# Optimization experiments

Measured on AMD Instinct MI355X. Metric: run time of the kernel, lower is better.

The kernel has to match this reference:

```python
import jax, jax.numpy as jnp
import numpy as np

D = 256; NH = 8; NL = 4; NP = 4; HD = D // NH
SHAPES = np.array([[64, 64], [32, 32], [16, 16], [8, 8]], dtype=np.int32)  # (H, W) per level
LSI = np.array([0, 4096, 5120, 5376], dtype=np.int32)
B = 4; LQ = int(SHAPES.prod(axis=1).sum())  # 5440


def setup_inputs() -> dict:
    key = jax.random.key(0)
    ks = jax.random.split(key, 16)
    p = lambda i, shape, s=0.02: jax.random.normal(ks[i], shape, dtype=jnp.float32) * s
    return dict(
        src=jax.random.normal(ks[0], (B, LQ, D), dtype=jnp.float32),
        pos=jax.random.normal(ks[1], (B, LQ, D), dtype=jnp.float32),
        reference_points=jax.random.uniform(ks[2], (B, LQ, NL, 2), dtype=jnp.float32),
        spatial_shapes=jnp.asarray(SHAPES),
        level_start_index=jnp.asarray(LSI),
        Wv=p(3, (D, D)), bv=jnp.zeros((D,), jnp.float32),
        Woff=p(4, (D, NH * NL * NP * 2)), boff=p(5, (NH * NL * NP * 2,)),
        Wattn=p(6, (D, NH * NL * NP)), battn=p(7, (NH * NL * NP,)),
        Wout=p(8, (D, D)), bout=jnp.zeros((D,), jnp.float32),
        g1=jnp.ones((D,), jnp.float32), b1=jnp.zeros((D,), jnp.float32),
        W1=p(9, (D, D)), bb1=jnp.zeros((D,), jnp.float32),
        W2=p(10, (D, D)), bb2=jnp.zeros((D,), jnp.float32),
        g3=jnp.ones((D,), jnp.float32), b3=jnp.zeros((D,), jnp.float32),
    )


def _ln(x, g, b, eps=1e-5):
    m = jnp.mean(x, -1, keepdims=True)
    v = jnp.mean(jnp.square(x - m), -1, keepdims=True)
    return (x - m) * jax.lax.rsqrt(v + eps) * g + b


def _bilinear(vflat, Hl, Wl, loc):
    # vflat: [B, Hl*Wl, nh, hd]; loc: [B, Lq, nh, np, 2] normalized to [0,1]
    # align_corners=False, zero padding (matches F.grid_sample in MSDeformAttn)
    x = loc[..., 0] * Wl - 0.5
    y = loc[..., 1] * Hl - 0.5
    x0 = jnp.floor(x); y0 = jnp.floor(y)
    fx = x - x0; fy = y - y0
    x0 = x0.astype(jnp.int32); y0 = y0.astype(jnp.int32)
    Bb, Lq, nh, npnt = x0.shape
    hd = vflat.shape[-1]
    out = jnp.zeros((Bb, Lq, nh, npnt, hd), vflat.dtype)
    for dy in (0, 1):
        for dx in (0, 1):
            xi = x0 + dx; yi = y0 + dy
            w = (fx if dx else 1.0 - fx) * (fy if dy else 1.0 - fy)
            valid = (xi >= 0) & (xi < Wl) & (yi >= 0) & (yi < Hl)
            idx = jnp.clip(yi, 0, Hl - 1) * Wl + jnp.clip(xi, 0, Wl - 1)  # [B,Lq,nh,np]
            idx = idx.transpose(0, 1, 3, 2).reshape(Bb, Lq * npnt, nh, 1)
            g = jnp.take_along_axis(vflat, idx, axis=1)
            g = g.reshape(Bb, Lq, npnt, nh, hd).transpose(0, 1, 3, 2, 4)
            out = out + g * (w * valid.astype(w.dtype))[..., None]
    return out  # [B, Lq, nh, np, hd]


def _forward(src, pos, reference_points, spatial_shapes, level_start_index,
             Wv, bv, Woff, boff, Wattn, battn, Wout, bout,
             g1, b1, W1, bb1, W2, bb2, g3, b3):
    shapes = np.asarray(spatial_shapes)
    lsi = np.asarray(level_start_index)
    Bq, Lq, Dm = src.shape
    q = src + pos  # with_pos_embed
    value = (src @ Wv + bv).reshape(Bq, Lq, NH, HD)
    off = (q @ Woff + boff).reshape(Bq, Lq, NH, NL, NP, 2)
    aw = jax.nn.softmax((q @ Wattn + battn).reshape(Bq, Lq, NH, NL * NP), axis=-1)
    aw = aw.reshape(Bq, Lq, NH, NL, NP)
    # offset normalizer is (W, H) per level
    norm = jnp.stack([shapes[:, 1].astype(np.float32), shapes[:, 0].astype(np.float32)], axis=-1)
    loc = reference_points[:, :, None, :, None, :] + off / norm[None, None, None, :, None, :]
    attended = jnp.zeros((Bq, Lq, NH, HD), src.dtype)
    for l in range(shapes.shape[0]):
        Hl, Wl = int(shapes[l, 0]), int(shapes[l, 1])
        s = int(lsi[l])
        vflat = value[:, s:s + Hl * Wl]
        sampled = _bilinear(vflat, Hl, Wl, loc[:, :, :, l])  # [B,Lq,nh,np,hd]
        attended = attended + jnp.einsum('blhpd,blhp->blhd', sampled, aw[:, :, :, l])
    src2 = attended.reshape(Bq, Lq, Dm) @ Wout + bout
    # residual + LayerNorm (dropout is identity in eval)
    sxy = _ln(src + src2, g1, b1)
    # FFN (d_ffn == d_model here), residual + LayerNorm
    h = jax.nn.relu(sxy @ W1 + bb1)
    return _ln(sxy + (h @ W2 + bb2), g3, b3)


def reference(src, pos, reference_points, spatial_shapes, level_start_index,
              Wv, bv, Woff, boff, Wattn, battn, Wout, bout,
              g1, b1, W1, bb1, W2, bb2, g3, b3):
    return _forward(src, pos, reference_points, spatial_shapes, level_start_index,
                    Wv, bv, Woff, boff, Wattn, battn, Wout, bout,
                    g1, b1, W1, bb1, W2, bb2, g3, b3)
```

## Files before the change

### kernel.cpp

```cpp
#include <hip/hip_runtime.h>
#include <cstddef>
#include <cstdint>

#define M_TOK 21760
#define LQ_ 5440

typedef _Float16 f16x8 __attribute__((ext_vector_type(8)));
typedef _Float16 h2v __attribute__((ext_vector_type(2)));
typedef float f32x4v __attribute__((ext_vector_type(4)));
typedef _Float16 half4v __attribute__((ext_vector_type(4)));

__device__ __forceinline__ unsigned short f2h(float f) {
  return __builtin_bit_cast(unsigned short, (_Float16)f);
}

__global__ __launch_bounds__(256) void prep_k(
    const float* __restrict__ src, const float* __restrict__ pos,
    const float* __restrict__ Wv, const float* __restrict__ Woff,
    const float* __restrict__ Wattn, const float* __restrict__ Wout,
    const float* __restrict__ W1, const float* __restrict__ W2,
    unsigned short* __restrict__ s16, unsigned short* __restrict__ q16,
    unsigned short* __restrict__ G)
{
  const int b = blockIdx.x;
  if (b < 5440) {
    const int i = b * 256 + threadIdx.x;
    const float4 s = ((const float4*)src)[i];
    const float4 p = ((const float4*)pos)[i];
    ushort4 a, q;
    a.x = f2h(s.x); a.y = f2h(s.y); a.z = f2h(s.z); a.w = f2h(s.w);
    q.x = f2h(s.x + p.x); q.y = f2h(s.y + p.y); q.z = f2h(s.z + p.z); q.w = f2h(s.w + p.w);
    ((ushort4*)s16)[i] = a;
    ((ushort4*)q16)[i] = q;
  } else {
    const int gid = (b - 5440) * 256 + threadIdx.x;
    const float* srcs[6] = {Wv, Woff, Wattn, Wout, W1, W2};
    const int starts[7] = {0, 65536, 131072, 163840, 229376, 294912, 360448};
    const int Nn[6] = {256, 256, 128, 256, 256, 256};
    int m = 0;
#pragma unroll
    for (int i = 1; i < 6; ++i) m += (gid >= starts[i]);
    const int local = gid - starts[m];
    const int n = local >> 8;
    const int k = local & 255;
    G[gid] = f2h(srcs[m][(size_t)k * Nn[m] + n]);
  }
}

__global__ __launch_bounds__(256, 2) void gemm_qkv_k(
    const unsigned short* __restrict__ s16, const unsigned short* __restrict__ q16,
    const unsigned short* __restrict__ WvT, const unsigned short* __restrict__ WfT,
    const float* __restrict__ bv, const float* __restrict__ boff,
    const float* __restrict__ battn,
    unsigned short* __restrict__ value16, unsigned short* __restrict__ fused16)
{
  const int by = blockIdx.y;
  const bool isv = (by < 2);
  const unsigned short* A  = isv ? s16 : q16;
  const unsigned short* Wt = isv ? WvT : WfT;
  const int n0 = isv ? by * 128 : (by - 2) * 128;
  const int N  = isv ? 256 : 384;
  unsigned short* out16 = isv ? value16 : fused16;
  const float* bsel; int nsub;
  if (isv)            { bsel = bv;    nsub = 0; }
  else if (n0 < 256)  { bsel = boff;  nsub = 0; }
  else                { bsel = battn; nsub = 256; }

  __shared__ unsigned short As[128 * 64];
  __shared__ unsigned short Bs[128 * 64];
  const int t = threadIdx.x;
  const int lane = t & 63, wave = t >> 6;
  const int wm = wave >> 1, wn = wave & 1;
  const int m0 = blockIdx.x * 128;

  const int lrow = lane >> 3;
  const int pcol = (lane & 7) << 4;
  const int scol = pcol ^ (lrow << 4);

  f32x4v acc[4][4];
#pragma unroll
  for (int i = 0; i < 4; ++i)
#pragma unroll
    for (int j = 0; j < 4; ++j) acc[i][j] = (f32x4v){0.f, 0.f, 0.f, 0.f};

  const int fr = lane & 15;
  const int fkb = (lane >> 4) << 4;

  for (int k0 = 0; k0 < 256; k0 += 64) {
#pragma unroll
    for (int i = 0; i < 4; ++i) {
      const int row = wave * 32 + i * 8 + lrow;
      const unsigned short* g = A + (size_t)(m0 + row) * 256 + k0 + (scol >> 1);
      unsigned short* s = As + (wave * 32 + i * 8) * 64;
      __builtin_amdgcn_global_load_lds(
          (const __attribute__((address_space(1))) void*)g,
          (__attribute__((address_space(3))) void*)s, 16, 0, 0);
    }
#pragma unroll
    for (int i = 0; i < 4; ++i) {
      const int row = wave * 32 + i * 8 + lrow;
      const unsigned short* g = Wt + (size_t)(n0 + row) * 256 + k0 + (scol >> 1);
      unsigned short* s = Bs + (wave * 32 + i * 8) * 64;
      __builtin_amdgcn_global_load_lds(
          (const __attribute__((address_space(1))) void*)g,
          (__attribute__((address_space(3))) void*)s, 16, 0, 0);
    }
    __syncthreads();

    f16x8 af[4][2], bfr[4][2];
#pragma unroll
    for (int i = 0; i < 4; ++i) {
      const int row = wm * 64 + i * 16 + fr;
      const char* base = (const char*)As + row * 128;
#pragma unroll
      for (int kk = 0; kk < 2; ++kk)
        af[i][kk] = *(const f16x8*)(base + ((kk * 64 + fkb) ^ ((row & 7) << 4)));
    }
#pragma unroll
    for (int j = 0; j < 4; ++j) {
      const int row = wn * 64 + j * 16 + fr;
      const char* base = (const char*)Bs + row * 128;
#pragma unroll
      for (int kk = 0; kk < 2; ++kk)
        bfr[j][kk] = *(const f16x8*)(base + ((kk * 64 + fkb) ^ ((row & 7) << 4)));
    }
#pragma unroll
    for (int i = 0; i < 4; ++i)
#pragma unroll
      for (int j = 0; j < 4; ++j) {
        acc[i][j] = __builtin_amdgcn_mfma_f32_16x16x32_f16(af[i][0], bfr[j][0], acc[i][j], 0, 0, 0);
        acc[i][j] = __builtin_amdgcn_mfma_f32_16x16x32_f16(af[i][1], bfr[j][1], acc[i][j], 0, 0, 0);
      }
    __syncthreads();
  }

  const int fq = lane >> 4;
#pragma unroll
  for (int j = 0; j < 4; ++j) {
    const int n = n0 + wn * 64 + j * 16 + fr;
    const float bj = bsel[n - nsub];
#pragma unroll
    for (int i = 0; i < 4; ++i) {
#pragma unroll
      for (int r = 0; r < 4; ++r) {
        const int m = m0 + wm * 64 + i * 16 + fq * 4 + r;
        out16[(size_t)m * N + n] = f2h(acc[i][j][r] + bj);
      }
    }
  }
}

__global__ __launch_bounds__(256, 2) void gemm16_k(
    const unsigned short* __restrict__ A, const unsigned short* __restrict__ Wt,
    const float* __restrict__ bias, unsigned short* __restrict__ out16,
    int N, int relu)
{
  __shared__ unsigned short As[128 * 64];
  __shared__ unsigned short Bs[128 * 64];
  const int t = threadIdx.x;
  const int lane = t & 63, wave = t >> 6;
  const int wm = wave >> 1, wn = wave & 1;
  const int m0 = blockIdx.x * 128, n0 = blockIdx.y * 128;

  const int lrow = lane >> 3;
  const int pcol = (lane & 7) << 4;
  const int scol = pcol ^ (lrow << 4);

  f32x4v acc[4][4];
#pragma unroll
  for (int i = 0; i < 4; ++i)
#pragma unroll
    for (int j = 0; j < 4; ++j) acc[i][j] = (f32x4v){0.f, 0.f, 0.f, 0.f};

  const int fr = lane & 15;
  const int fkb = (lane >> 4) << 4;

  for (int k0 = 0; k0 < 256; k0 += 64) {
#pragma unroll
    for (int i = 0; i < 4; ++i) {
      const int row = wave * 32 + i * 8 + lrow;
      const unsigned short* g = A + (size_t)(m0 + row) * 256 + k0 + (scol >> 1);
      unsigned short* s = As + (wave * 32 + i * 8) * 64;
      __builtin_amdgcn_global_load_lds(
          (const __attribute__((address_space(1))) void*)g,
          (__attribute__((address_space(3))) void*)s, 16, 0, 0);
    }
#pragma unroll
    for (int i = 0; i < 4; ++i) {
      const int row = wave * 32 + i * 8 + lrow;
      const unsigned short* g = Wt + (size_t)(n0 + row) * 256 + k0 + (scol >> 1);
      unsigned short* s = Bs + (wave * 32 + i * 8) * 64;
      __builtin_amdgcn_global_load_lds(
          (const __attribute__((address_space(1))) void*)g,
          (__attribute__((address_space(3))) void*)s, 16, 0, 0);
    }
    __syncthreads();

    f16x8 af[4][2], bfr[4][2];
#pragma unroll
    for (int i = 0; i < 4; ++i) {
      const int row = wm * 64 + i * 16 + fr;
      const char* base = (const char*)As + row * 128;
#pragma unroll
      for (int kk = 0; kk < 2; ++kk)
        af[i][kk] = *(const f16x8*)(base + ((kk * 64 + fkb) ^ ((row & 7) << 4)));
    }
#pragma unroll
    for (int j = 0; j < 4; ++j) {
      const int row = wn * 64 + j * 16 + fr;
      const char* base = (const char*)Bs + row * 128;
#pragma unroll
      for (int kk = 0; kk < 2; ++kk)
        bfr[j][kk] = *(const f16x8*)(base + ((kk * 64 + fkb) ^ ((row & 7) << 4)));
    }
#pragma unroll
    for (int i = 0; i < 4; ++i)
#pragma unroll
      for (int j = 0; j < 4; ++j) {
        acc[i][j] = __builtin_amdgcn_mfma_f32_16x16x32_f16(af[i][0], bfr[j][0], acc[i][j], 0, 0, 0);
        acc[i][j] = __builtin_amdgcn_mfma_f32_16x16x32_f16(af[i][1], bfr[j][1], acc[i][j], 0, 0, 0);
      }
    __syncthreads();
  }

  const int fq = lane >> 4;
#pragma unroll
  for (int j = 0; j < 4; ++j) {
    const int n = n0 + wn * 64 + j * 16 + fr;
    const float bj = bias[n];
#pragma unroll
    for (int i = 0; i < 4; ++i) {
#pragma unroll
      for (int r = 0; r < 4; ++r) {
        const int m = m0 + wm * 64 + i * 16 + fq * 4 + r;
        float v = acc[i][j][r] + bj;
        if (relu) v = fmaxf(v, 0.f);
        out16[(size_t)m * N + n] = f2h(v);
      }
    }
  }
}

__global__ __launch_bounds__(512, 4) void gemm_ln_k(
    const unsigned short* __restrict__ A, const unsigned short* __restrict__ Wt,
    const float* __restrict__ bias, const float* __restrict__ res,
    const float* __restrict__ g, const float* __restrict__ b,
    float* __restrict__ outf, unsigned short* __restrict__ out16)
{
  __shared__ unsigned short As[32 * 64];
  __shared__ unsigned short Bs[256 * 64 + 288];
  const int t = threadIdx.x;
  const int lane = t & 63, wave = t >> 6;
  const int rt = wave & 1, cg = wave >> 1;
  const int m0 = blockIdx.x * 32;

  const int lrow = lane >> 3;
  const int pcol = (lane & 7) << 4;
  const int scol = pcol ^ (lrow << 4);

  f32x4v acc[4];
#pragma unroll
  for (int j = 0; j < 4; ++j) acc[j] = (f32x4v){0.f, 0.f, 0.f, 0.f};

  const int fr = lane & 15;
  const int fq = lane >> 4;
  const int fkb = fq << 4;

  for (int k0 = 0; k0 < 256; k0 += 64) {
    if (wave < 4) {
      const int row = wave * 8 + lrow;
      const unsigned short* gp = A + (size_t)(m0 + row) * 256 + k0 + (scol >> 1);
      unsigned short* s = As + (wave * 8) * 64;
      __builtin_amdgcn_global_load_lds(
          (const __attribute__((address_space(1))) void*)gp,
          (__attribute__((address_space(3))) void*)s, 16, 0, 0);
    }
#pragma unroll
    for (int i = 0; i < 4; ++i) {
      const int row = wave * 32 + i * 8 + lrow;
      const unsigned short* gp = Wt + (size_t)row * 256 + k0 + (scol >> 1);
      unsigned short* s = Bs + (wave * 32 + i * 8) * 64;
      __builtin_amdgcn_global_load_lds(
          (const __attribute__((address_space(1))) void*)gp,
          (__attribute__((address_space(3))) void*)s, 16, 0, 0);
    }
    __syncthreads();

    f16x8 af0, af1;
    {
      const int arow = rt * 16 + fr;
      const char* abase = (const char*)As + arow * 128;
      af0 = *(const f16x8*)(abase + ((0 + fkb) ^ ((arow & 7) << 4)));
      af1 = *(const f16x8*)(abase + ((64 + fkb) ^ ((arow & 7) << 4)));
    }
#pragma unroll
    for (int j = 0; j < 4; ++j) {
      const int brow = cg * 64 + j * 16 + fr;
      const char* bbase = (const char*)Bs + brow * 128;
      const f16x8 b0 = *(const f16x8*)(bbase + ((0 + fkb) ^ ((brow & 7) << 4)));
      const f16x8 b1 = *(const f16x8*)(bbase + ((64 + fkb) ^ ((brow & 7) << 4)));
      acc[j] = __builtin_amdgcn_mfma_f32_16x16x32_f16(af0, b0, acc[j], 0, 0, 0);
      acc[j] = __builtin_amdgcn_mfma_f32_16x16x32_f16(af1, b1, acc[j], 0, 0, 0);
    }
    __syncthreads();
  }

  float* Cs = (float*)Bs;
#pragma unroll
  for (int j = 0; j < 4; ++j) {
    const int col = cg * 64 + j * 16 + fr;
#pragma unroll
    for (int rr = 0; rr < 4; ++rr) {
      const int row = rt * 16 + fq * 4 + rr;
      Cs[row * 260 + col] = acc[j][rr];
    }
  }
  __syncthreads();

  const int lg = lane >> 4, li = lane & 15;
  const int row = wave * 4 + lg;
  const size_t rowoff = (size_t)(m0 + row) * 256;

  float4 v[4];
  float s = 0.f;
#pragma unroll
  for (int c4 = 0; c4 < 4; ++c4) {
    const int col = c4 * 64 + li * 4;
    float4 x = *(float4*)&Cs[row * 260 + col];
    const float4 bi = *(const float4*)&bias[col];
    const float4 rv = *(const float4*)&res[rowoff + col];
    x.x += bi.x + rv.x; x.y += bi.y + rv.y;
    x.z += bi.z + rv.z; x.w += bi.w + rv.w;
    v[c4] = x;
    s += x.x + x.y + x.z + x.w;
  }
#pragma unroll
  for (int o = 1; o < 16; o <<= 1) s += __shfl_xor(s, o);
  const float mean = s * (1.f / 256.f);
  float ss = 0.f;
#pragma unroll
  for (int c4 = 0; c4 < 4; ++c4) {
    const float d0 = v[c4].x - mean, d1 = v[c4].y - mean;
    const float d2 = v[c4].z - mean, d3 = v[c4].w - mean;
    ss += d0 * d0 + d1 * d1 + d2 * d2 + d3 * d3;
  }
#pragma unroll
  for (int o = 1; o < 16; o <<= 1) ss += __shfl_xor(ss, o);
  const float rstd = rsqrtf(ss * (1.f / 256.f) + 1e-5f);

#pragma unroll
  for (int c4 = 0; c4 < 4; ++c4) {
    const int col = c4 * 64 + li * 4;
    const float4 gv = *(const float4*)&g[col];
    const float4 bv = *(const float4*)&b[col];
    float4 o4;
    o4.x = (v[c4].x - mean) * rstd * gv.x + bv.x;
    o4.y = (v[c4].y - mean) * rstd * gv.y + bv.y;
    o4.z = (v[c4].z - mean) * rstd * gv.z + bv.z;
    o4.w = (v[c4].w - mean) * rstd * gv.w + bv.w;
    if (outf) *(float4*)(outf + rowoff + col) = o4;
    if (out16) {
      ushort4 o;
      o.x = f2h(o4.x); o.y = f2h(o4.y); o.z = f2h(o4.z); o.w = f2h(o4.w);
      *(ushort4*)(out16 + rowoff + col) = o;
    }
  }
}

__global__ __launch_bounds__(256) void samp_k(
    const unsigned short* __restrict__ value16, const unsigned short* __restrict__ fused16,
    const float* __restrict__ ref, unsigned short* __restrict__ att16)
{
  const int tok0 = blockIdx.x * 8;
  __shared__ half4v swv[8][136];
  __shared__ int4   siv[8][136];
  const int t = threadIdx.x;
  const _Float16* fh = (const _Float16*)fused16;

#pragma unroll
  for (int it = 0; it < 4; ++it) {
    const int idx = it * 256 + t;
    const int ti = idx >> 7;
    const int e  = idx & 127;
    const int tok = tok0 + ti;
    const int h = e >> 4;
    const int lvl = (e >> 2) & 3;
    const int HW[4] = {64, 32, 16, 8};
    const int LS[4] = {0, 4096, 5120, 5376};
    const int Wl = HW[lvl];

    const float lg = (float)fh[(size_t)tok * 384 + 256 + e];
    float mx = lg;
#pragma unroll
    for (int o = 1; o < 16; o <<= 1) mx = fmaxf(mx, __shfl_xor(mx, o, 16));
    const float ex = __expf(lg - mx);
    float sm = ex;
#pragma unroll
    for (int o = 1; o < 16; o <<= 1) sm += __shfl_xor(sm, o, 16);
    const float a = ex / sm;

    const float ox = (float)fh[(size_t)tok * 384 + e * 2 + 0];
    const float oy = (float)fh[(size_t)tok * 384 + e * 2 + 1];
    const float rx = ref[(size_t)tok * 8 + lvl * 2 + 0];
    const float ry = ref[(size_t)tok * 8 + lvl * 2 + 1];
    const float x = rx * (float)Wl + ox - 0.5f;
    const float y = ry * (float)Wl + oy - 0.5f;
    const float x0f = floorf(x), y0f = floorf(y);
    const float fx = x - x0f, fy = y - y0f;
    const int x0 = (int)x0f, y0 = (int)y0f;

    const int xi1 = x0 + 1, yi1 = y0 + 1;
    const float wx0 = 1.f - fx, wx1 = fx, wy0 = 1.f - fy, wy1 = fy;
    const int xc0 = min(max(x0, 0), Wl - 1), xc1 = min(max(xi1, 0), Wl - 1);
    const int yc0 = min(max(y0, 0), Wl - 1), yc1 = min(max(yi1, 0), Wl - 1);
    const bool vx0 = (x0 >= 0) & (x0 < Wl), vx1 = (xi1 >= 0) & (xi1 < Wl);
    const bool vy0 = (y0 >= 0) & (y0 < Wl), vy1 = (yi1 >= 0) & (yi1 < Wl);
    half4v hw;
    hw.x = (_Float16)((vx0 & vy0) ? a * wx0 * wy0 : 0.f);
    hw.y = (_Float16)((vx1 & vy0) ? a * wx1 * wy0 : 0.f);
    hw.z = (_Float16)((vx0 & vy1) ? a * wx0 * wy1 : 0.f);
    hw.w = (_Float16)((vx1 & vy1) ? a * wx1 * wy1 : 0.f);
    int4 io;
    io.x = (LS[lvl] + yc0 * Wl + xc0) << 9;
    io.y = (LS[lvl] + yc0 * Wl + xc1) << 9;
    io.z = (LS[lvl] + yc1 * Wl + xc0) << 9;
    io.w = (LS[lvl] + yc1 * Wl + xc1) << 9;
    const int sl = e + h;
    swv[ti][sl] = hw;
    siv[ti][sl] = io;
  }
  __syncthreads();

  const int wave = t >> 6, lane = t & 63;
  const int ti = wave * 2 + (lane >> 5);
  const int h = (lane >> 2) & 7, dg = lane & 3;
  const int tok = tok0 + ti;
  const int vbase = (tok0 / LQ_) * LQ_;
  const char* vb = (const char*)(value16 + (size_t)vbase * 256);
  const int laneoff = h * 64 + dg * 16;
  h2v a0 = {0, 0}, a1 = {0, 0}, a2 = {0, 0}, a3 = {0, 0};
  const int ebase = h * 17;

#pragma unroll 4
  for (int p = 0; p < 16; ++p) {
    const half4v hw = swv[ti][ebase + p];
    const int4 io = siv[ti][ebase + p];
    const uint4 u0 = *(const uint4*)(vb + (io.x + laneoff));
    const uint4 u1 = *(const uint4*)(vb + (io.y + laneoff));
    const uint4 u2 = *(const uint4*)(vb + (io.z + laneoff));
    const uint4 u3 = *(const uint4*)(vb + (io.w + laneoff));
#define CORNER(U, WI) {                                            \
    const h2v w2 = __builtin_shufflevector(hw, hw, WI, WI);        \
    a0 += w2 * __builtin_bit_cast(h2v, U.x);                       \
    a1 += w2 * __builtin_bit_cast(h2v, U.y);                       \
    a2 += w2 * __builtin_bit_cast(h2v, U.z);                       \
    a3 += w2 * __builtin_bit_cast(h2v, U.w); }
    CORNER(u0, 0) CORNER(u1, 1) CORNER(u2, 2) CORNER(u3, 3)
#undef CORNER
  }

  uint4 o;
  o.x = __builtin_bit_cast(unsigned, a0);
  o.y = __builtin_bit_cast(unsigned, a1);
  o.z = __builtin_bit_cast(unsigned, a2);
  o.w = __builtin_bit_cast(unsigned, a3);
  *(uint4*)(att16 + (size_t)tok * 256 + h * 32 + dg * 8) = o;
}

extern "C" void kernel_launch(void* const* d_in, const int* in_sizes, int n_in,
                              void* d_out, int out_size, void* d_ws, size_t ws_size,
                              hipStream_t stream)
{
  const float* src   = (const float*)d_in[0];
  const float* pos   = (const float*)d_in[1];
  const float* ref   = (const float*)d_in[2];
  const float* Wv    = (const float*)d_in[5];
  const float* bv    = (const float*)d_in[6];
  const float* Woff  = (const float*)d_in[7];
  const float* boff  = (const float*)d_in[8];
  const float* Wattn = (const float*)d_in[9];
  const float* battn = (const float*)d_in[10];
  const float* Wout  = (const float*)d_in[11];
  const float* bout  = (const float*)d_in[12];
  const float* g1    = (const float*)d_in[13];
  const float* b1    = (const float*)d_in[14];
  const float* W1    = (const float*)d_in[15];
  const float* bb1   = (const float*)d_in[16];
  const float* W2    = (const float*)d_in[17];
  const float* bb2   = (const float*)d_in[18];
  const float* g3    = (const float*)d_in[19];
  const float* b3    = (const float*)d_in[20];

  float* out = (float*)d_out;
  char* ws = (char*)d_ws;
  const size_t M = M_TOK;

  float* bufA = (float*)ws;
  unsigned short* fused16 = (unsigned short*)(ws + M * 256 * 4);
  unsigned short* bufE = fused16 + M * 384;
  unsigned short* bufF = bufE + M * 256;
  unsigned short* bufG = bufF + M * 256;
  unsigned short* value16 = (unsigned short*)bufA;

  unsigned short* WvT     = bufG + 0;
  unsigned short* WfusedT = bufG + 65536;
  unsigned short* WoutT   = bufG + 163840;
  unsigned short* W1T     = bufG + 229376;
  unsigned short* W2T     = bufG + 294912;

  const dim3 blk(256);

  prep_k<<<dim3(6848), blk, 0, stream>>>(src, pos, Wv, Woff, Wattn, Wout, W1, W2,
                                         bufE, bufF, bufG);
  gemm_qkv_k<<<dim3(170, 5), blk, 0, stream>>>(bufE, bufF, WvT, WfusedT,
                                               bv, boff, battn, value16, fused16);
  samp_k<<<dim3(2720), blk, 0, stream>>>(value16, fused16, ref, bufE);
  gemm_ln_k<<<dim3(680), dim3(512), 0, stream>>>(bufE, WoutT, bout, src, g1, b1, bufA, bufF);
  gemm16_k<<<dim3(170, 2), blk, 0, stream>>>(bufF, W1T, bb1, bufE, 256, 1);
  gemm_ln_k<<<dim3(680), dim3(512), 0, stream>>>(bufE, W2T, bb2, bufA, g3, b3, out, nullptr);
}
```

Baseline: 105.2 us.

## Use padded value buffer to drop x-clamping and share corner indices in sampler

The value buffer is moved 1 KB into the workspace, and zeroed guard rows are written before and after it. The sampler can then store only two row base offsets per point: the clamp on x is relaxed to -1, and the right corner is read at +512 bytes, with out-of-range corners carrying zero weight. This halves the shared-memory index storage and the address arithmetic. The gather loop is fully unrolled two points at a time to put more loads in flight, blocks are remapped so batches interleave, and occupancy is hinted at 6 blocks per CU. The risk is that an x0=-1 or x1=Wl read lands in a neighbouring row or the pad, which is only correct because those corners are zero-weighted. The added guard-row zeroing must also stay outside the bufA region that is reused later.

```diff
diff --git a/kernel.cpp b/kernel.cpp
--- a/kernel.cpp
+++ b/kernel.cpp
@@ -20,7 +20,7 @@
     const float* __restrict__ Wattn, const float* __restrict__ Wout,
     const float* __restrict__ W1, const float* __restrict__ W2,
     unsigned short* __restrict__ s16, unsigned short* __restrict__ q16,
-    unsigned short* __restrict__ G)
+    unsigned short* __restrict__ G, char* __restrict__ wsbase)
 {
   const int b = blockIdx.x;
   if (b < 5440) {
@@ -32,7 +32,7 @@
     q.x = f2h(s.x + p.x); q.y = f2h(s.y + p.y); q.z = f2h(s.z + p.z); q.w = f2h(s.w + p.w);
     ((ushort4*)s16)[i] = a;
     ((ushort4*)q16)[i] = q;
-  } else {
+  } else if (b < 6848) {
     const int gid = (b - 5440) * 256 + threadIdx.x;
     const float* srcs[6] = {Wv, Woff, Wattn, Wout, W1, W2};
     const int starts[7] = {0, 65536, 131072, 163840, 229376, 294912, 360448};
@@ -44,6 +44,14 @@
     const int n = local >> 8;
     const int k = local & 255;
     G[gid] = f2h(srcs[m][(size_t)k * Nn[m] + n]);
+  } else {
+    const int tid = threadIdx.x;
+    const uint4 z = {0u, 0u, 0u, 0u};
+    if (tid < 64) {
+      ((uint4*)wsbase)[tid] = z;
+    } else if (tid < 128) {
+      ((uint4*)(wsbase + 1024 + (size_t)M_TOK * 512))[tid - 64] = z;
+    }
   }
 }
 
@@ -367,13 +375,16 @@
   }
 }
 
-__global__ __launch_bounds__(256) void samp_k(
+__global__ __launch_bounds__(256, 6) void samp_k(
     const unsigned short* __restrict__ value16, const unsigned short* __restrict__ fused16,
     const float* __restrict__ ref, unsigned short* __restrict__ att16)
 {
-  const int tok0 = blockIdx.x * 8;
+  const int b = blockIdx.x;
+  const int wg = (b & 7) * 340 + (b >> 3);
+  const int tok0 = wg * 8;
+
   __shared__ half4v swv[8][136];
-  __shared__ int4   siv[8][136];
+  __shared__ int2   siv[8][136];
   const int t = threadIdx.x;
   const _Float16* fh = (const _Float16*)fused16;
 
@@ -411,8 +422,6 @@
 
     const int xi1 = x0 + 1, yi1 = y0 + 1;
     const float wx0 = 1.f - fx, wx1 = fx, wy0 = 1.f - fy, wy1 = fy;
-    const int xc0 = min(max(x0, 0), Wl - 1), xc1 = min(max(xi1, 0), Wl - 1);
-    const int yc0 = min(max(y0, 0), Wl - 1), yc1 = min(max(yi1, 0), Wl - 1);
     const bool vx0 = (x0 >= 0) & (x0 < Wl), vx1 = (xi1 >= 0) & (xi1 < Wl);
     const bool vy0 = (y0 >= 0) & (y0 < Wl), vy1 = (yi1 >= 0) & (yi1 < Wl);
     half4v hw;
@@ -420,11 +429,12 @@
     hw.y = (_Float16)((vx1 & vy0) ? a * wx1 * wy0 : 0.f);
     hw.z = (_Float16)((vx0 & vy1) ? a * wx0 * wy1 : 0.f);
     hw.w = (_Float16)((vx1 & vy1) ? a * wx1 * wy1 : 0.f);
-    int4 io;
-    io.x = (LS[lvl] + yc0 * Wl + xc0) << 9;
-    io.y = (LS[lvl] + yc0 * Wl + xc1) << 9;
-    io.z = (LS[lvl] + yc1 * Wl + xc0) << 9;
-    io.w = (LS[lvl] + yc1 * Wl + xc1) << 9;
+    const int ax  = min(max(x0, -1), Wl - 1);
+    const int yc0 = min(max(y0, 0), Wl - 1);
+    const int yc1 = min(max(yi1, 0), Wl - 1);
+    int2 io;
+    io.x = (LS[lvl] + yc0 * Wl + ax) << 9;
+    io.y = (LS[lvl] + yc1 * Wl + ax) << 9;
     const int sl = e + h;
     swv[ti][sl] = hw;
     siv[ti][sl] = io;
@@ -441,23 +451,35 @@
   h2v a0 = {0, 0}, a1 = {0, 0}, a2 = {0, 0}, a3 = {0, 0};
   const int ebase = h * 17;
 
-#pragma unroll 4
-  for (int p = 0; p < 16; ++p) {
-    const half4v hw = swv[ti][ebase + p];
-    const int4 io = siv[ti][ebase + p];
-    const uint4 u0 = *(const uint4*)(vb + (io.x + laneoff));
-    const uint4 u1 = *(const uint4*)(vb + (io.y + laneoff));
-    const uint4 u2 = *(const uint4*)(vb + (io.z + laneoff));
-    const uint4 u3 = *(const uint4*)(vb + (io.w + laneoff));
-#define CORNER(U, WI) {                                            \
-    const h2v w2 = __builtin_shufflevector(hw, hw, WI, WI);        \
+#define CORNER(U, HW_, WI) {                                       \
+    const h2v w2 = __builtin_shufflevector(HW_, HW_, WI, WI);      \
     a0 += w2 * __builtin_bit_cast(h2v, U.x);                       \
     a1 += w2 * __builtin_bit_cast(h2v, U.y);                       \
     a2 += w2 * __builtin_bit_cast(h2v, U.z);                       \
     a3 += w2 * __builtin_bit_cast(h2v, U.w); }
-    CORNER(u0, 0) CORNER(u1, 1) CORNER(u2, 2) CORNER(u3, 3)
+
+#pragma unroll
+  for (int p = 0; p < 16; p += 2) {
+    const half4v w0 = swv[ti][ebase + p];
+    const half4v w1 = swv[ti][ebase + p + 1];
+    const int2 i0 = siv[ti][ebase + p];
+    const int2 i1 = siv[ti][ebase + p + 1];
+    const char* p00 = vb + (i0.x + laneoff);
+    const char* p01 = vb + (i0.y + laneoff);
+    const char* p10 = vb + (i1.x + laneoff);
+    const char* p11 = vb + (i1.y + laneoff);
+    const uint4 u0 = *(const uint4*)(p00);
+    const uint4 u1 = *(const uint4*)(p00 + 512);
+    const uint4 u2 = *(const uint4*)(p01);
+    const uint4 u3 = *(const uint4*)(p01 + 512);
+    const uint4 u4 = *(const uint4*)(p10);
+    const uint4 u5 = *(const uint4*)(p10 + 512);
+    const uint4 u6 = *(const uint4*)(p11);
+    const uint4 u7 = *(const uint4*)(p11 + 512);
+    CORNER(u0, w0, 0) CORNER(u1, w0, 1) CORNER(u2, w0, 2) CORNER(u3, w0, 3)
+    CORNER(u4, w1, 0) CORNER(u5, w1, 1) CORNER(u6, w1, 2) CORNER(u7, w1, 3)
+  }
 #undef CORNER
-  }
 
   uint4 o;
   o.x = __builtin_bit_cast(unsigned, a0);
@@ -500,7 +522,7 @@
   unsigned short* bufE = fused16 + M * 384;
   unsigned short* bufF = bufE + M * 256;
   unsigned short* bufG = bufF + M * 256;
-  unsigned short* value16 = (unsigned short*)bufA;
+  unsigned short* value16 = (unsigned short*)(ws + 1024);
 
   unsigned short* WvT     = bufG + 0;
   unsigned short* WfusedT = bufG + 65536;
@@ -510,8 +532,8 @@
 
   const dim3 blk(256);
 
-  prep_k<<<dim3(6848), blk, 0, stream>>>(src, pos, Wv, Woff, Wattn, Wout, W1, W2,
-                                         bufE, bufF, bufG);
+  prep_k<<<dim3(6849), blk, 0, stream>>>(src, pos, Wv, Woff, Wattn, Wout, W1, W2,
+                                         bufE, bufF, bufG, ws);
   gemm_qkv_k<<<dim3(170, 5), blk, 0, stream>>>(bufE, bufF, WvT, WfusedT,
                                                bv, boff, battn, value16, fused16);
   samp_k<<<dim3(2720), blk, 0, stream>>>(value16, fused16, ref, bufE);
```

New measurement: 105.3 us. No clear change (+0.2%).
